# Kernel tuning notes

Measured on AMD Instinct MI355X. Metric: run time of the kernel, lower is better.

## Reference

```python
import jax, jax.numpy as jnp
import numpy as np

B = 2048
F = 267          # frame_size
L = 32           # latent_size
H = 256          # hidden_size (hard-coded in module)
E = 8            # num_experts
G = 64           # gate hidden size (hard-coded)
IN0 = L + F      # decoder layer0 input (latent + frame*cond_frames)
IN1 = L + H      # decoder inter input
OUT = F          # num_future_predictions * frame_size


def _lin_init(key, out_dim, in_dim):
    # kaiming-uniform-like scale
    bound = float(np.sqrt(1.0 / in_dim))
    return jax.random.uniform(key, (out_dim, in_dim), jnp.float32, -bound, bound)


def setup_inputs() -> dict:
    key = jax.random.key(0)
    ks = jax.random.split(key, 24)
    d = {}
    d["x"] = jax.random.normal(ks[0], (B, F), jnp.float32)
    d["c"] = jax.random.normal(ks[1], (B, F), jnp.float32)
    # encoder
    d["fc1_w"] = _lin_init(ks[2], H, 2 * F); d["fc1_b"] = jnp.zeros((H,), jnp.float32)
    d["fc2_w"] = _lin_init(ks[3], H, F + H); d["fc2_b"] = jnp.zeros((H,), jnp.float32)
    d["mu_w"] = _lin_init(ks[4], L, F + H);  d["mu_b"] = jnp.zeros((L,), jnp.float32)
    d["lv_w"] = _lin_init(ks[5], L, F + H);  d["lv_b"] = jnp.zeros((L,), jnp.float32)
    # gate
    d["g0_w"] = _lin_init(ks[6], G, IN0); d["g0_b"] = jnp.zeros((G,), jnp.float32)
    d["g1_w"] = _lin_init(ks[7], G, G);   d["g1_b"] = jnp.zeros((G,), jnp.float32)
    d["g2_w"] = _lin_init(ks[8], E, G);   d["g2_b"] = jnp.zeros((E,), jnp.float32)
    # expert weights [E, in, out], biases [E, out], bias filled 0.01 as in module
    d["w0"] = jax.random.uniform(ks[9], (E, IN0, H), jnp.float32, -1, 1) * np.sqrt(1.0 / IN0)
    d["b0"] = jnp.full((E, H), 0.01, jnp.float32)
    d["w1"] = jax.random.uniform(ks[10], (E, IN1, H), jnp.float32, -1, 1) * np.sqrt(1.0 / IN1)
    d["b1"] = jnp.full((E, H), 0.01, jnp.float32)
    d["w2"] = jax.random.uniform(ks[11], (E, IN1, OUT), jnp.float32, -1, 1) * np.sqrt(1.0 / IN1)
    d["b2"] = jnp.full((E, OUT), 0.01, jnp.float32)
    return d


def reference(x, c, fc1_w, fc1_b, fc2_w, fc2_b, mu_w, mu_b, lv_w, lv_b,
              g0_w, g0_b, g1_w, g1_b, g2_w, g2_b, w0, b0, w1, b1, w2, b2):
    elu = jax.nn.elu
    # ---- encoder ----
    h1 = elu(jnp.concatenate([x, c], axis=1) @ fc1_w.T + fc1_b)
    h2 = elu(jnp.concatenate([x, h1], axis=1) @ fc2_w.T + fc2_b)
    s = jnp.concatenate([x, h2], axis=1)
    mu = s @ mu_w.T + mu_b
    logvar = s @ lv_w.T + lv_b
    eps = jax.random.normal(jax.random.key(42), mu.shape, mu.dtype)
    z = mu + eps * jnp.exp(0.5 * logvar)
    # ---- mixed decoder ----
    g = elu(jnp.concatenate([z, c], axis=1) @ g0_w.T + g0_b)
    g = elu(g @ g1_w.T + g1_b)
    coeff = jax.nn.softmax(g @ g2_w.T + g2_b, axis=1)  # [B, E]
    layer_out = c
    for (W, bvec, act) in ((w0, b0, True), (w1, b1, True), (w2, b2, False)):
        inp = jnp.concatenate([z, layer_out], axis=1)          # [B, in]
        # per-expert GEMM then coefficient mixing (same math as per-sample
        # mixed-weight bmm: coeff @ flat_weight then baddbmm)
        out = jnp.einsum('be,bi,eio->bo', coeff, inp, W, optimize=True)
        out = out + coeff @ bvec                               # mixed bias
        layer_out = elu(out) if act else out
    return (layer_out, mu, logvar)
```

## Files before the change

### kernel.cpp

```cpp
#include <hip/hip_runtime.h>
#include <math.h>
#include <stdint.h>

#define DI __device__ __forceinline__

typedef __attribute__((ext_vector_type(8))) short bf16x8;
typedef __attribute__((ext_vector_type(4))) float f32x4;
typedef __attribute__((ext_vector_type(4))) int i32x4;

DI float elu_f(float v) { return v > 0.f ? v : expm1f(v); }

DI unsigned short f2bf(float f) {
  uint32_t u = __float_as_uint(f);
  return (unsigned short)((u + 0x7FFFu + ((u >> 16) & 1u)) >> 16);
}

DI void threefry2x32(uint32_t k0, uint32_t k1, uint32_t& x0, uint32_t& x1) {
  uint32_t ks0 = k0, ks1 = k1, ks2 = k0 ^ k1 ^ 0x1BD11BDAu;
  x0 += ks0; x1 += ks1;
#define TFR(r) { x0 += x1; x1 = (x1 << r) | (x1 >> (32 - r)); x1 ^= x0; }
  TFR(13) TFR(15) TFR(26) TFR(6)   x0 += ks1; x1 += ks2 + 1u;
  TFR(17) TFR(29) TFR(16) TFR(24)  x0 += ks2; x1 += ks0 + 2u;
  TFR(13) TFR(15) TFR(26) TFR(6)   x0 += ks0; x1 += ks1 + 3u;
  TFR(17) TFR(29) TFR(16) TFR(24)  x0 += ks1; x1 += ks2 + 4u;
  TFR(13) TFR(15) TFR(26) TFR(6)   x0 += ks2; x1 += ks0 + 5u;
#undef TFR
}

DI float erfinv_f(float x) {
  float w = -logf((1.0f - x) * (1.0f + x));
  float p;
  if (w < 5.0f) {
    w -= 2.5f;
    p = 2.81022636e-08f;
    p = fmaf(p, w, 3.43273939e-07f);
    p = fmaf(p, w, -3.5233877e-06f);
    p = fmaf(p, w, -4.39150654e-06f);
    p = fmaf(p, w, 0.00021858087f);
    p = fmaf(p, w, -0.00125372503f);
    p = fmaf(p, w, -0.00417768164f);
    p = fmaf(p, w, 0.246640727f);
    p = fmaf(p, w, 1.50140941f);
  } else {
    w = sqrtf(w) - 3.0f;
    p = -0.000200214257f;
    p = fmaf(p, w, 0.000100950558f);
    p = fmaf(p, w, 0.00134934322f);
    p = fmaf(p, w, -0.00367342844f);
    p = fmaf(p, w, 0.00573950773f);
    p = fmaf(p, w, -0.0076224613f);
    p = fmaf(p, w, 0.00943887047f);
    p = fmaf(p, w, 1.00167406f);
    p = fmaf(p, w, 2.83297682f);
  }
  return p * x;
}

struct MegaArgs {
  const float *x, *c;
  const float *fc1w, *fc1b, *fc2w, *fc2b, *muw, *mub, *lvw, *lvb;
  const float *g0w, *g0b, *g1w, *g1b, *g2w, *g2b;
  const float *w0, *b0, *w1, *b1, *w2, *b2;
  unsigned short *Ax, *Axh, *Axh2, *A0, *A1, *A2;
  unsigned short *fc1t, *fc2t, *mlvt, *g0t, *g1t, *w0b, *w1b, *w2b;
  float *cf, *outY, *outMu, *outLv;
};

template <int KT, int NE, int D, bool ELU, bool OUTF32>
__global__ __launch_bounds__(128, 2)
void pipe16(const unsigned short* __restrict__ A,
            const unsigned short* __restrict__ Wt, int N,
            const float* __restrict__ bias,
            const float* __restrict__ cfp,
            unsigned short* __restrict__ Cb, int ldcb, int cb_off,
            float* __restrict__ Cf) {
  constexpr int Kp = KT * 32, TT = NE * KT;
  __shared__ float bias_s[NE * 16];
  __shared__ float cfs[(NE > 1) ? 256 : 1];
  const int tid = threadIdx.x, lane = tid & 63, wid = tid >> 6;
  const int q = lane >> 4, l16 = lane & 15;
  const int m0 = blockIdx.x * 32, n0 = blockIdx.y * 16;
  const int gc = n0 + l16;
  const int wrow = (gc < N) ? gc : (N - 1);
  const unsigned short* wlane = Wt + (size_t)wrow * Kp + q * 8;
  const unsigned short* alane = A + (size_t)(m0 + wid * 16 + l16) * Kp + q * 8;

  bf16x8 ring[D];
#pragma unroll
  for (int g = 0; g < D; g++) {
    if (g < TT) {
      int e = g / KT, c = g % KT;
      ring[g] = *(const bf16x8*)(wlane + (size_t)e * N * Kp + c * 32);
    }
  }
  bf16x8 areg[KT];
#pragma unroll
  for (int c = 0; c < KT; c++) areg[c] = *(const bf16x8*)(alane + c * 32);

  if (NE == 1) {
    if (tid < 16) bias_s[tid] = (n0 + tid < N) ? bias[n0 + tid] : 0.f;
  } else {
    if (tid < NE * 16) {
      int e = tid >> 4, col = tid & 15;
      bias_s[tid] = (n0 + col < N) ? bias[(size_t)e * N + n0 + col] : 0.f;
    }
    for (int idx = tid; idx < 256; idx += 128)
      cfs[idx] = cfp[(size_t)(m0 + (idx >> 3)) * 8 + (idx & 7)];
  }
  __syncthreads();

  f32x4 acc = {0.f, 0.f, 0.f, 0.f}, accF = {0.f, 0.f, 0.f, 0.f};
#pragma unroll
  for (int g = 0; g < TT; g++) {
    const int e = g / KT, c = g % KT;
    acc = __builtin_amdgcn_mfma_f32_16x16x32_bf16(areg[c], ring[g % D], acc, 0, 0, 0);
    if (g + D < TT) {
      int e2 = (g + D) / KT, c2 = (g + D) % KT;
      ring[g % D] = *(const bf16x8*)(wlane + (size_t)e2 * N * Kp + c2 * 32);
    }
    if (NE > 1 && c == KT - 1) {
      float bv2 = bias_s[e * 16 + l16];
#pragma unroll
      for (int r = 0; r < 4; r++) {
        float ce = cfs[(wid * 16 + q * 4 + r) * 8 + e];
        accF[r] += ce * (acc[r] + bv2);
        acc[r] = 0.f;
      }
    }
  }

  if (gc < N) {
#pragma unroll
    for (int r = 0; r < 4; r++) {
      int row = m0 + wid * 16 + q * 4 + r;
      float v = (NE > 1) ? accF[r] : (acc[r] + bias_s[l16]);
      if (ELU) v = elu_f(v);
      if (OUTF32) Cf[(size_t)row * 267 + gc] = v;
      else Cb[(size_t)row * ldcb + cb_off + gc] = f2bf(v);
    }
  }
}

__global__ __launch_bounds__(256) void k_prep(MegaArgs a) {
  __shared__ __align__(16) unsigned short T[64][72];
  const int bb = blockIdx.x, tid = threadIdx.x;
  if (bb < 512) {
    for (int rr = 0; rr < 4; rr++) {
      int b = bb * 4 + rr;
      const float* xr = a.x + (size_t)b * 267;
      const float* cr = a.c + (size_t)b * 267;
      unsigned short* axr = a.Ax + (size_t)b * 544;
      for (int k = tid; k < 544; k += 256) {
        float v = (k < 267) ? xr[k] : ((k < 534) ? cr[k - 267] : 0.f);
        axr[k] = f2bf(v);
      }
      unsigned short* ahr = a.Axh + (size_t)b * 544;
      unsigned short* ah2 = a.Axh2 + (size_t)b * 544;
      for (int k = tid; k < 267; k += 256) { unsigned short v = f2bf(xr[k]); ahr[k] = v; ah2[k] = v; }
      for (int k = 523 + tid; k < 544; k += 256) { ahr[k] = 0; ah2[k] = 0; }
      unsigned short* a0r = a.A0 + (size_t)b * 320;
      for (int k = tid; k < 288; k += 256)
        a0r[32 + k] = (k < 267) ? f2bf(cr[k]) : (unsigned short)0;
    }
  } else if (bb < 1152) {
    int r = bb - 512;
    const float* src; unsigned short* dst; int Ks, Kp2;
    if (r < 256)      { src = a.fc1w + (size_t)r * 534; dst = a.fc1t + (size_t)r * 544; Ks = 534; Kp2 = 544; }
    else if (r < 512) { int n = r - 256; src = a.fc2w + (size_t)n * 523; dst = a.fc2t + (size_t)n * 544; Ks = 523; Kp2 = 544; }
    else if (r < 576) { int n = r - 512; src = (n < 32) ? (a.muw + (size_t)n * 523) : (a.lvw + (size_t)(n - 32) * 523);
                        dst = a.mlvt + (size_t)n * 544; Ks = 523; Kp2 = 544; }
    else              { int n = r - 576; src = a.g0w + (size_t)n * 299; dst = a.g0t + (size_t)n * 320; Ks = 299; Kp2 = 320; }
    for (int k = tid; k < Kp2; k += 256) dst[k] = (k < Ks) ? f2bf(src[k]) : (unsigned short)0;
  } else if (bb == 1152) {
    for (int k = tid; k < 4096; k += 256) a.g1t[k] = f2bf(a.g1w[k]);
  } else {
    int t = bb - 1153;
    const float* W; unsigned short* D; int K, N2, Kp2, ldW, e, kt, nt;
    if (t < 160)      { e = t / 20;  int lt = t % 20;  kt = lt / 4; nt = lt % 4; W = a.w0; D = a.w0b; K = 299; N2 = 256; Kp2 = 320; ldW = 256; }
    else if (t < 320) { int u = t - 160; e = u / 20; int lt = u % 20; kt = lt / 4; nt = lt % 4; W = a.w1; D = a.w1b; K = 288; N2 = 256; Kp2 = 288; ldW = 256; }
    else              { int u = t - 320; e = u / 25; int lt = u % 25; kt = lt / 5; nt = lt % 5; W = a.w2; D = a.w2b; K = 288; N2 = 267; Kp2 = 288; ldW = 267; }
    const int k0 = kt * 64, n0 = nt * 64;
    const float* We = W + (size_t)e * K * ldW;
    const int jj = tid & 63, ii0 = tid >> 6;
#pragma unroll
    for (int p = 0; p < 16; p++) {
      int i = ii0 + p * 4;
      int gk = k0 + i, gn = n0 + jj;
      float v = (gk < K && gn < N2) ? We[(size_t)gk * ldW + gn] : 0.f;
      T[jj][i] = f2bf(v);
    }
    __syncthreads();
    int j = tid >> 2, chb = tid & 3;
    int gn = n0 + j;
    if (gn < N2) {
      unsigned short* drow = D + ((size_t)e * N2 + gn) * Kp2 + k0;
#pragma unroll
      for (int s = 0; s < 2; s++) {
        int ch = chb + s * 4;
        if (k0 + ch * 8 < Kp2) {
          i32x4 v = *(i32x4*)(&T[j][ch * 8]);
          *(i32x4*)(drow + ch * 8) = v;
        }
      }
    }
  }
}

__global__ __launch_bounds__(256, 2) void k_mulv_gate(MegaArgs a) {
  __shared__ float mlvS[16 * 65];
  __shared__ __align__(16) unsigned short A0p[16 * 328];
  __shared__ __align__(16) unsigned short gaB[16 * 72];
  __shared__ __align__(16) unsigned short g1B[64 * 72];
  __shared__ float g2wT[64 * 8];
  __shared__ float gB[16 * 65];
  __shared__ float lg[16 * 8];
  const int tid = threadIdx.x, lane = tid & 63, wid = tid >> 6;
  const int q = lane >> 4, l16 = lane & 15;
  const int m0 = blockIdx.x * 16;
  const int cl = wid * 16 + l16;

  const unsigned short* alane = a.Axh2 + (size_t)(m0 + l16) * 544 + q * 8;
  const unsigned short* wlA = a.mlvt + (size_t)cl * 544 + q * 8;
  bf16x8 ring[8];
#pragma unroll
  for (int g = 0; g < 8; g++) ring[g] = *(const bf16x8*)(wlA + g * 32);
  bf16x8 areg[17];
#pragma unroll
  for (int c = 0; c < 17; c++) areg[c] = *(const bf16x8*)(alane + c * 32);
  f32x4 acc = {0.f, 0.f, 0.f, 0.f};
#pragma unroll
  for (int g = 0; g < 17; g++) {
    acc = __builtin_amdgcn_mfma_f32_16x16x32_bf16(areg[g], ring[g % 8], acc, 0, 0, 0);
    if (g + 8 < 17) ring[g % 8] = *(const bf16x8*)(wlA + (g + 8) * 32);
  }
#pragma unroll
  for (int r = 0; r < 4; r++) mlvS[(q * 4 + r) * 65 + cl] = acc[r];
  for (int idx = tid; idx < 576; idx += 256) {
    int row = idx / 36, ch = 4 + idx % 36;
    *(i32x4*)(A0p + row * 328 + ch * 8) =
        *(const i32x4*)(a.A0 + (size_t)(m0 + row) * 320 + ch * 8);
  }
  if (tid < 16) { i32x4 z4 = {0, 0, 0, 0}; *(i32x4*)(A0p + tid * 328 + 320) = z4; }
  for (int idx = tid; idx < 512; idx += 256) {
    int row = idx >> 3, ch = idx & 7;
    *(i32x4*)(g1B + row * 72 + ch * 8) = *(const i32x4*)(a.g1t + (size_t)row * 64 + ch * 8);
  }
  for (int idx = tid; idx < 512; idx += 256)
    g2wT[(idx & 63) * 8 + (idx >> 6)] = a.g2w[idx];
  __syncthreads();

  {
    const int m = tid >> 4, j0 = (tid & 15) * 2, R = m0 + m;
#pragma unroll
    for (int jj = 0; jj < 2; jj++) {
      int j = j0 + jj;
      float mu = mlvS[m * 65 + j] + a.mub[j];
      float lvv = mlvS[m * 65 + j + 32] + a.lvb[j];
      uint32_t x0 = 0u, x1 = (uint32_t)(R * 32 + j);
      threefry2x32(0u, 42u, x0, x1);
      uint32_t bits = x0 ^ x1;
      float f = __uint_as_float((bits >> 9) | 0x3F800000u) - 1.0f;
      const float lo = -0.99999994039535522461f;
      float u = fmaf(f, 2.0f, lo);
      u = fmaxf(u, lo);
      float eps = 1.41421356237f * erfinv_f(u);
      float z = fmaf(eps, expf(0.5f * lvv), mu);
      a.outMu[(size_t)R * 32 + j] = mu;
      a.outLv[(size_t)R * 32 + j] = lvv;
      unsigned short zb = f2bf(z);
      A0p[m * 328 + j] = zb;
      a.A0[(size_t)R * 320 + j] = zb;
      a.A1[(size_t)R * 288 + j] = zb;
      a.A2[(size_t)R * 288 + j] = zb;
    }
  }
  __syncthreads();

  const unsigned short* wlC = a.g0t + (size_t)cl * 320 + q * 8;
  bf16x8 ring2[8];
#pragma unroll
  for (int g = 0; g < 8; g++) ring2[g] = *(const bf16x8*)(wlC + g * 32);
  f32x4 accC = {0.f, 0.f, 0.f, 0.f};
#pragma unroll
  for (int g = 0; g < 10; g++) {
    bf16x8 av = *(const bf16x8*)(A0p + l16 * 328 + g * 32 + q * 8);
    accC = __builtin_amdgcn_mfma_f32_16x16x32_bf16(av, ring2[g % 8], accC, 0, 0, 0);
    if (g + 8 < 10) ring2[g % 8] = *(const bf16x8*)(wlC + (g + 8) * 32);
  }
  {
    float bc = a.g0b[cl];
#pragma unroll
    for (int r = 0; r < 4; r++)
      gaB[(q * 4 + r) * 72 + cl] = f2bf(elu_f(accC[r] + bc));
  }
  __syncthreads();

  f32x4 accD = {0.f, 0.f, 0.f, 0.f};
#pragma unroll
  for (int tau = 0; tau < 2; tau++) {
    bf16x8 av = *(const bf16x8*)(gaB + l16 * 72 + tau * 32 + q * 8);
    bf16x8 bv = *(const bf16x8*)(g1B + cl * 72 + tau * 32 + q * 8);
    accD = __builtin_amdgcn_mfma_f32_16x16x32_bf16(av, bv, accD, 0, 0, 0);
  }
  {
    float bc = a.g1b[cl];
#pragma unroll
    for (int r = 0; r < 4; r++)
      gB[(q * 4 + r) * 65 + cl] = elu_f(accD[r] + bc);
  }
  __syncthreads();

  if (tid < 128) {
    int r = tid >> 3, e = tid & 7;
    float d = a.g2b[e];
#pragma unroll 8
    for (int k = 0; k < 64; k++) d = fmaf(gB[r * 65 + k], g2wT[k * 8 + e], d);
    lg[r * 8 + e] = d;
  }
  __syncthreads();
  if (tid < 16) {
    float mx = lg[tid * 8];
#pragma unroll
    for (int e2 = 1; e2 < 8; e2++) mx = fmaxf(mx, lg[tid * 8 + e2]);
    float s = 0.f, ex[8];
#pragma unroll
    for (int e2 = 0; e2 < 8; e2++) { ex[e2] = expf(lg[tid * 8 + e2] - mx); s += ex[e2]; }
    float inv = 1.f / s;
#pragma unroll
    for (int e2 = 0; e2 < 8; e2++) a.cf[(size_t)(m0 + tid) * 8 + e2] = ex[e2] * inv;
  }
}

extern "C" void kernel_launch(void* const* d_in, const int* in_sizes, int n_in,
                              void* d_out, int out_size, void* d_ws, size_t ws_size,
                              hipStream_t stream) {
  (void)in_sizes; (void)n_in; (void)out_size; (void)ws_size;
  float* out = (float*)d_out;
  float* ws = (float*)d_ws;

  MegaArgs a;
  a.x    = (const float*)d_in[0];
  a.c    = (const float*)d_in[1];
  a.fc1w = (const float*)d_in[2];  a.fc1b = (const float*)d_in[3];
  a.fc2w = (const float*)d_in[4];  a.fc2b = (const float*)d_in[5];
  a.muw  = (const float*)d_in[6];  a.mub  = (const float*)d_in[7];
  a.lvw  = (const float*)d_in[8];  a.lvb  = (const float*)d_in[9];
  a.g0w  = (const float*)d_in[10]; a.g0b  = (const float*)d_in[11];
  a.g1w  = (const float*)d_in[12]; a.g1b  = (const float*)d_in[13];
  a.g2w  = (const float*)d_in[14]; a.g2b  = (const float*)d_in[15];
  a.w0   = (const float*)d_in[16]; a.b0   = (const float*)d_in[17];
  a.w1   = (const float*)d_in[18]; a.b1   = (const float*)d_in[19];
  a.w2   = (const float*)d_in[20]; a.b2   = (const float*)d_in[21];

  a.outY  = out;
  a.outMu = out + 2048 * 267;
  a.outLv = a.outMu + 2048 * 32;

  a.Ax   = (unsigned short*)(ws);
  a.Axh  = (unsigned short*)(ws + 557056);
  a.Axh2 = (unsigned short*)(ws + 1114112);
  a.A0   = (unsigned short*)(ws + 1671168);
  a.A1   = (unsigned short*)(ws + 1998848);
  a.A2   = (unsigned short*)(ws + 2293760);
  a.fc1t = (unsigned short*)(ws + 2588672);
  a.fc2t = (unsigned short*)(ws + 2658304);
  a.mlvt = (unsigned short*)(ws + 2727936);
  a.g0t  = (unsigned short*)(ws + 2745344);
  a.g1t  = (unsigned short*)(ws + 2755584);
  a.w0b  = (unsigned short*)(ws + 2757632);
  a.w1b  = (unsigned short*)(ws + 3085312);
  a.w2b  = (unsigned short*)(ws + 3380224);
  a.cf   = ws + 3687808;

  dim3 blkP(256), blkG(128);
  k_prep<<<1673, blkP, 0, stream>>>(a);
  pipe16<17, 1, 12, true, false><<<dim3(64, 16), blkG, 0, stream>>>(
      a.Ax, a.fc1t, 256, a.fc1b, nullptr, a.Axh, 544, 267, nullptr);
  pipe16<17, 1, 12, true, false><<<dim3(64, 16), blkG, 0, stream>>>(
      a.Axh, a.fc2t, 256, a.fc2b, nullptr, a.Axh2, 544, 267, nullptr);
  k_mulv_gate<<<128, blkP, 0, stream>>>(a);
  pipe16<10, 8, 16, true, false><<<dim3(64, 16), blkG, 0, stream>>>(
      a.A0, a.w0b, 256, a.b0, a.cf, a.A1, 288, 32, nullptr);
  pipe16<9, 8, 16, true, false><<<dim3(64, 16), blkG, 0, stream>>>(
      a.A1, a.w1b, 256, a.b1, a.cf, a.A2, 288, 32, nullptr);
  pipe16<9, 8, 16, false, true><<<dim3(64, 17), blkG, 0, stream>>>(
      a.A2, a.w2b, 267, a.b2, a.cf, nullptr, 0, 0, a.outY);
}
```

Measured before the change: 182.8 us.

## Fuse encoder, gate and expert decoder into one per-row-block kernel

```diff
diff --git a/kernel.cpp b/kernel.cpp
--- a/kernel.cpp
+++ b/kernel.cpp
@@ -61,198 +61,153 @@
   const float *fc1w, *fc1b, *fc2w, *fc2b, *muw, *mub, *lvw, *lvb;
   const float *g0w, *g0b, *g1w, *g1b, *g2w, *g2b;
   const float *w0, *b0, *w1, *b1, *w2, *b2;
-  unsigned short *Ax, *Axh, *Axh2, *A0, *A1, *A2;
   unsigned short *fc1t, *fc2t, *mlvt, *g0t, *g1t, *w0b, *w1b, *w2b;
-  float *cf, *outY, *outMu, *outLv;
+  float *outY, *outMu, *outLv;
 };
 
-template <int KT, int NE, int D, bool ELU, bool OUTF32>
-__global__ __launch_bounds__(128, 2)
-void pipe16(const unsigned short* __restrict__ A,
-            const unsigned short* __restrict__ Wt, int N,
-            const float* __restrict__ bias,
-            const float* __restrict__ cfp,
-            unsigned short* __restrict__ Cb, int ldcb, int cb_off,
-            float* __restrict__ Cf) {
-  constexpr int Kp = KT * 32, TT = NE * KT;
-  __shared__ float bias_s[NE * 16];
-  __shared__ float cfs[(NE > 1) ? 256 : 1];
-  const int tid = threadIdx.x, lane = tid & 63, wid = tid >> 6;
+template <int KT, int NE, int TPW, int MODE>
+DI void seg(int lane,
+            const unsigned short* AL, int ldA,
+            const unsigned short* __restrict__ Wt, int N, int tbase,
+            const float* __restrict__ biasG, const float* cfsL,
+            unsigned short* outB, int ldOB, int coffB,
+            float* outF, int ldOF) {
+  constexpr int Kp = KT * 32, D = 8, TT = TPW * NE * KT;
   const int q = lane >> 4, l16 = lane & 15;
-  const int m0 = blockIdx.x * 32, n0 = blockIdx.y * 16;
-  const int gc = n0 + l16;
-  const int wrow = (gc < N) ? gc : (N - 1);
-  const unsigned short* wlane = Wt + (size_t)wrow * Kp + q * 8;
-  const unsigned short* alane = A + (size_t)(m0 + wid * 16 + l16) * Kp + q * 8;
-
+  bf16x8 areg[KT];
+#pragma unroll
+  for (int c = 0; c < KT; c++)
+    areg[c] = *(const bf16x8*)(AL + l16 * ldA + c * 32 + q * 8);
+  int gc[TPW];
+  const unsigned short* wl[TPW];
+  float br[TPW][NE];
+  float cfr[(NE > 1) ? NE * 4 : 1];
+#pragma unroll
+  for (int t = 0; t < TPW; t++) {
+    gc[t] = tbase + t * 16 + l16;
+    int wr = (gc[t] < N) ? gc[t] : N - 1;
+    wl[t] = Wt + (size_t)wr * Kp + q * 8;
+    if (MODE != 1) {
+#pragma unroll
+      for (int e = 0; e < NE; e++)
+        br[t][e] = (gc[t] < N) ? biasG[(size_t)e * N + gc[t]] : 0.f;
+    }
+  }
+  if (NE > 1) {
+#pragma unroll
+    for (int e = 0; e < NE; e++)
+#pragma unroll
+      for (int r = 0; r < 4; r++)
+        cfr[e * 4 + r] = cfsL[(q * 4 + r) * 8 + e];
+  }
   bf16x8 ring[D];
 #pragma unroll
   for (int g = 0; g < D; g++) {
     if (g < TT) {
-      int e = g / KT, c = g % KT;
-      ring[g] = *(const bf16x8*)(wlane + (size_t)e * N * Kp + c * 32);
-    }
-  }
-  bf16x8 areg[KT];
-#pragma unroll
-  for (int c = 0; c < KT; c++) areg[c] = *(const bf16x8*)(alane + c * 32);
-
-  if (NE == 1) {
-    if (tid < 16) bias_s[tid] = (n0 + tid < N) ? bias[n0 + tid] : 0.f;
-  } else {
-    if (tid < NE * 16) {
-      int e = tid >> 4, col = tid & 15;
-      bias_s[tid] = (n0 + col < N) ? bias[(size_t)e * N + n0 + col] : 0.f;
-    }
-    for (int idx = tid; idx < 256; idx += 128)
-      cfs[idx] = cfp[(size_t)(m0 + (idx >> 3)) * 8 + (idx & 7)];
-  }
-  __syncthreads();
-
-  f32x4 acc = {0.f, 0.f, 0.f, 0.f}, accF = {0.f, 0.f, 0.f, 0.f};
+      int t = g / (NE * KT), e = (g / KT) % NE, c = g % KT;
+      ring[g] = *(const bf16x8*)(wl[t] + (size_t)e * N * Kp + c * 32);
+    }
+  }
+  f32x4 acc[TPW], accF[TPW];
+#pragma unroll
+  for (int t = 0; t < TPW; t++) {
+    acc[t] = {0.f, 0.f, 0.f, 0.f};
+    accF[t] = {0.f, 0.f, 0.f, 0.f};
+  }
 #pragma unroll
   for (int g = 0; g < TT; g++) {
-    const int e = g / KT, c = g % KT;
-    acc = __builtin_amdgcn_mfma_f32_16x16x32_bf16(areg[c], ring[g % D], acc, 0, 0, 0);
+    const int t = g / (NE * KT), e = (g / KT) % NE, c = g % KT;
+    acc[t] = __builtin_amdgcn_mfma_f32_16x16x32_bf16(areg[c], ring[g % D], acc[t], 0, 0, 0);
     if (g + D < TT) {
-      int e2 = (g + D) / KT, c2 = (g + D) % KT;
-      ring[g % D] = *(const bf16x8*)(wlane + (size_t)e2 * N * Kp + c2 * 32);
+      int t2 = (g + D) / (NE * KT), e2 = ((g + D) / KT) % NE, c2 = (g + D) % KT;
+      ring[g % D] = *(const bf16x8*)(wl[t2] + (size_t)e2 * N * Kp + c2 * 32);
     }
     if (NE > 1 && c == KT - 1) {
-      float bv2 = bias_s[e * 16 + l16];
 #pragma unroll
       for (int r = 0; r < 4; r++) {
-        float ce = cfs[(wid * 16 + q * 4 + r) * 8 + e];
-        accF[r] += ce * (acc[r] + bv2);
-        acc[r] = 0.f;
+        accF[t][r] += cfr[e * 4 + r] * (acc[t][r] + br[t][e]);
+        acc[t][r] = 0.f;
       }
     }
   }
-
-  if (gc < N) {
+#pragma unroll
+  for (int t = 0; t < TPW; t++) {
+    if (gc[t] >= N) continue;
 #pragma unroll
     for (int r = 0; r < 4; r++) {
-      int row = m0 + wid * 16 + q * 4 + r;
-      float v = (NE > 1) ? accF[r] : (acc[r] + bias_s[l16]);
-      if (ELU) v = elu_f(v);
-      if (OUTF32) Cf[(size_t)row * 267 + gc] = v;
-      else Cb[(size_t)row * ldcb + cb_off + gc] = f2bf(v);
-    }
-  }
-}
-
-__global__ __launch_bounds__(256) void k_prep(MegaArgs a) {
-  __shared__ __align__(16) unsigned short T[64][72];
-  const int bb = blockIdx.x, tid = threadIdx.x;
-  if (bb < 512) {
-    for (int rr = 0; rr < 4; rr++) {
-      int b = bb * 4 + rr;
-      const float* xr = a.x + (size_t)b * 267;
-      const float* cr = a.c + (size_t)b * 267;
-      unsigned short* axr = a.Ax + (size_t)b * 544;
-      for (int k = tid; k < 544; k += 256) {
-        float v = (k < 267) ? xr[k] : ((k < 534) ? cr[k - 267] : 0.f);
-        axr[k] = f2bf(v);
-      }
-      unsigned short* ahr = a.Axh + (size_t)b * 544;
-      unsigned short* ah2 = a.Axh2 + (size_t)b * 544;
-      for (int k = tid; k < 267; k += 256) { unsigned short v = f2bf(xr[k]); ahr[k] = v; ah2[k] = v; }
-      for (int k = 523 + tid; k < 544; k += 256) { ahr[k] = 0; ah2[k] = 0; }
-      unsigned short* a0r = a.A0 + (size_t)b * 320;
-      for (int k = tid; k < 288; k += 256)
-        a0r[32 + k] = (k < 267) ? f2bf(cr[k]) : (unsigned short)0;
-    }
-  } else if (bb < 1152) {
-    int r = bb - 512;
-    const float* src; unsigned short* dst; int Ks, Kp2;
-    if (r < 256)      { src = a.fc1w + (size_t)r * 534; dst = a.fc1t + (size_t)r * 544; Ks = 534; Kp2 = 544; }
-    else if (r < 512) { int n = r - 256; src = a.fc2w + (size_t)n * 523; dst = a.fc2t + (size_t)n * 544; Ks = 523; Kp2 = 544; }
-    else if (r < 576) { int n = r - 512; src = (n < 32) ? (a.muw + (size_t)n * 523) : (a.lvw + (size_t)(n - 32) * 523);
-                        dst = a.mlvt + (size_t)n * 544; Ks = 523; Kp2 = 544; }
-    else              { int n = r - 576; src = a.g0w + (size_t)n * 299; dst = a.g0t + (size_t)n * 320; Ks = 299; Kp2 = 320; }
-    for (int k = tid; k < Kp2; k += 256) dst[k] = (k < Ks) ? f2bf(src[k]) : (unsigned short)0;
-  } else if (bb == 1152) {
-    for (int k = tid; k < 4096; k += 256) a.g1t[k] = f2bf(a.g1w[k]);
-  } else {
-    int t = bb - 1153;
-    const float* W; unsigned short* D; int K, N2, Kp2, ldW, e, kt, nt;
-    if (t < 160)      { e = t / 20;  int lt = t % 20;  kt = lt / 4; nt = lt % 4; W = a.w0; D = a.w0b; K = 299; N2 = 256; Kp2 = 320; ldW = 256; }
-    else if (t < 320) { int u = t - 160; e = u / 20; int lt = u % 20; kt = lt / 4; nt = lt % 4; W = a.w1; D = a.w1b; K = 288; N2 = 256; Kp2 = 288; ldW = 256; }
-    else              { int u = t - 320; e = u / 25; int lt = u % 25; kt = lt / 5; nt = lt % 5; W = a.w2; D = a.w2b; K = 288; N2 = 267; Kp2 = 288; ldW = 267; }
-    const int k0 = kt * 64, n0 = nt * 64;
-    const float* We = W + (size_t)e * K * ldW;
-    const int jj = tid & 63, ii0 = tid >> 6;
-#pragma unroll
-    for (int p = 0; p < 16; p++) {
-      int i = ii0 + p * 4;
-      int gk = k0 + i, gn = n0 + jj;
-      float v = (gk < K && gn < N2) ? We[(size_t)gk * ldW + gn] : 0.f;
-      T[jj][i] = f2bf(v);
-    }
-    __syncthreads();
-    int j = tid >> 2, chb = tid & 3;
-    int gn = n0 + j;
-    if (gn < N2) {
-      unsigned short* drow = D + ((size_t)e * N2 + gn) * Kp2 + k0;
-#pragma unroll
-      for (int s = 0; s < 2; s++) {
-        int ch = chb + s * 4;
-        if (k0 + ch * 8 < Kp2) {
-          i32x4 v = *(i32x4*)(&T[j][ch * 8]);
-          *(i32x4*)(drow + ch * 8) = v;
-        }
-      }
-    }
-  }
-}
-
-__global__ __launch_bounds__(256, 2) void k_mulv_gate(MegaArgs a) {
-  __shared__ float mlvS[16 * 65];
-  __shared__ __align__(16) unsigned short A0p[16 * 328];
-  __shared__ __align__(16) unsigned short gaB[16 * 72];
-  __shared__ __align__(16) unsigned short g1B[64 * 72];
-  __shared__ float g2wT[64 * 8];
-  __shared__ float gB[16 * 65];
-  __shared__ float lg[16 * 8];
-  const int tid = threadIdx.x, lane = tid & 63, wid = tid >> 6;
-  const int q = lane >> 4, l16 = lane & 15;
+      const int row = q * 4 + r;
+      if (MODE == 0)
+        outB[row * ldOB + coffB + gc[t]] = f2bf(elu_f(acc[t][r] + br[t][0]));
+      else if (MODE == 1)
+        outF[row * ldOF + gc[t]] = acc[t][r];
+      else if (MODE == 4)
+        outF[row * ldOF + gc[t]] = elu_f(acc[t][r] + br[t][0]);
+      else if (MODE == 2)
+        outB[row * ldOB + coffB + gc[t]] = f2bf(elu_f(accF[t][r]));
+      else
+        outF[(size_t)row * ldOF + gc[t]] = accF[t][r];
+    }
+  }
+}
+
+__global__ __launch_bounds__(512, 2) void row_net(MegaArgs a) {
+  __shared__ __align__(16) unsigned char SM[46336];
+  unsigned short* Acat0 = (unsigned short*)SM;
+  unsigned short* Acat1 = (unsigned short*)(SM + 17664);
+  unsigned short* A0p   = (unsigned short*)(SM + 35328);
+  float* cfs = (float*)(SM + 45824);
+  unsigned short* A1p = Acat0;
+  float* gB   = (float*)(SM + 9472);
+  float* lg   = (float*)(SM + 13632);
+  float* g2wT = (float*)(SM + 14144);
+  unsigned short* A2p = Acat1;
+  float* mlvS = (float*)(SM + 17664 + 9472);
+  unsigned short* gaB = (unsigned short*)(SM + 17664 + 13632);
+
+  const int tid = threadIdx.x, lane = tid & 63, wv = tid >> 6;
   const int m0 = blockIdx.x * 16;
-  const int cl = wid * 16 + l16;
-
-  const unsigned short* alane = a.Axh2 + (size_t)(m0 + l16) * 544 + q * 8;
-  const unsigned short* wlA = a.mlvt + (size_t)cl * 544 + q * 8;
-  bf16x8 ring[8];
-#pragma unroll
-  for (int g = 0; g < 8; g++) ring[g] = *(const bf16x8*)(wlA + g * 32);
-  bf16x8 areg[17];
-#pragma unroll
-  for (int c = 0; c < 17; c++) areg[c] = *(const bf16x8*)(alane + c * 32);
-  f32x4 acc = {0.f, 0.f, 0.f, 0.f};
-#pragma unroll
-  for (int g = 0; g < 17; g++) {
-    acc = __builtin_amdgcn_mfma_f32_16x16x32_bf16(areg[g], ring[g % 8], acc, 0, 0, 0);
-    if (g + 8 < 17) ring[g % 8] = *(const bf16x8*)(wlA + (g + 8) * 32);
-  }
-#pragma unroll
-  for (int r = 0; r < 4; r++) mlvS[(q * 4 + r) * 65 + cl] = acc[r];
-  for (int idx = tid; idx < 576; idx += 256) {
-    int row = idx / 36, ch = 4 + idx % 36;
-    *(i32x4*)(A0p + row * 328 + ch * 8) =
-        *(const i32x4*)(a.A0 + (size_t)(m0 + row) * 320 + ch * 8);
-  }
-  if (tid < 16) { i32x4 z4 = {0, 0, 0, 0}; *(i32x4*)(A0p + tid * 328 + 320) = z4; }
-  for (int idx = tid; idx < 512; idx += 256) {
-    int row = idx >> 3, ch = idx & 7;
-    *(i32x4*)(g1B + row * 72 + ch * 8) = *(const i32x4*)(a.g1t + (size_t)row * 64 + ch * 8);
-  }
-  for (int idx = tid; idx < 512; idx += 256)
-    g2wT[(idx & 63) * 8 + (idx >> 6)] = a.g2w[idx];
-  __syncthreads();
-
-  {
-    const int m = tid >> 4, j0 = (tid & 15) * 2, R = m0 + m;
-#pragma unroll
-    for (int jj = 0; jj < 2; jj++) {
+
+  for (int idx = tid; idx < 16 * 267; idx += 512) {
+    int r = idx / 267, k = idx % 267;
+    unsigned short xv = f2bf(a.x[(size_t)(m0 + r) * 267 + k]);
+    Acat0[r * 552 + k] = xv;
+    Acat1[r * 552 + k] = xv;
+    unsigned short cv = f2bf(a.c[(size_t)(m0 + r) * 267 + k]);
+    Acat0[r * 552 + 267 + k] = cv;
+    A0p[r * 328 + 32 + k] = cv;
+  }
+  for (int idx = tid; idx < 16 * 18; idx += 512) {
+    int r = idx / 18, k = idx % 18;
+    Acat0[r * 552 + 534 + k] = 0;
+  }
+  for (int idx = tid; idx < 16 * 29; idx += 512) {
+    int r = idx / 29, k = idx % 29;
+    Acat1[r * 552 + 523 + k] = 0;
+  }
+  for (int idx = tid; idx < 16 * 29; idx += 512) {
+    int r = idx / 29, k = idx % 29;
+    A0p[r * 328 + 299 + k] = 0;
+  }
+  __syncthreads();
+
+  seg<17, 1, 2, 0>(lane, Acat0, 552, a.fc1t, 256, wv * 32, a.fc1b, nullptr,
+                   Acat1, 552, 267, nullptr, 0);
+  __syncthreads();
+  seg<17, 1, 2, 0>(lane, Acat1, 552, a.fc2t, 256, wv * 32, a.fc2b, nullptr,
+                   Acat0, 552, 267, nullptr, 0);
+  for (int idx = tid; idx < 16 * 21; idx += 512) {
+    int r = idx / 21, k = idx % 21;
+    Acat0[r * 552 + 523 + k] = 0;
+  }
+  __syncthreads();
+  if (wv < 4)
+    seg<17, 1, 1, 1>(lane, Acat0, 552, a.mlvt, 64, wv * 16, nullptr, nullptr,
+                     nullptr, 0, 0, mlvS, 65);
+  __syncthreads();
+  if (tid < 128) {
+    const int m = tid >> 3, j0 = (tid & 7) * 4, R = m0 + m;
+#pragma unroll
+    for (int jj = 0; jj < 4; jj++) {
       int j = j0 + jj;
       float mu = mlvS[m * 65 + j] + a.mub[j];
       float lvv = mlvS[m * 65 + j + 32] + a.lvb[j];
@@ -269,47 +224,23 @@
       a.outLv[(size_t)R * 32 + j] = lvv;
       unsigned short zb = f2bf(z);
       A0p[m * 328 + j] = zb;
-      a.A0[(size_t)R * 320 + j] = zb;
-      a.A1[(size_t)R * 288 + j] = zb;
-      a.A2[(size_t)R * 288 + j] = zb;
-    }
-  }
-  __syncthreads();
-
-  const unsigned short* wlC = a.g0t + (size_t)cl * 320 + q * 8;
-  bf16x8 ring2[8];
-#pragma unroll
-  for (int g = 0; g < 8; g++) ring2[g] = *(const bf16x8*)(wlC + g * 32);
-  f32x4 accC = {0.f, 0.f, 0.f, 0.f};
-#pragma unroll
-  for (int g = 0; g < 10; g++) {
-    bf16x8 av = *(const bf16x8*)(A0p + l16 * 328 + g * 32 + q * 8);
-    accC = __builtin_amdgcn_mfma_f32_16x16x32_bf16(av, ring2[g % 8], accC, 0, 0, 0);
-    if (g + 8 < 10) ring2[g % 8] = *(const bf16x8*)(wlC + (g + 8) * 32);
-  }
-  {
-    float bc = a.g0b[cl];
-#pragma unroll
-    for (int r = 0; r < 4; r++)
-      gaB[(q * 4 + r) * 72 + cl] = f2bf(elu_f(accC[r] + bc));
-  }
-  __syncthreads();
-
-  f32x4 accD = {0.f, 0.f, 0.f, 0.f};
-#pragma unroll
-  for (int tau = 0; tau < 2; tau++) {
-    bf16x8 av = *(const bf16x8*)(gaB + l16 * 72 + tau * 32 + q * 8);
-    bf16x8 bv = *(const bf16x8*)(g1B + cl * 72 + tau * 32 + q * 8);
-    accD = __builtin_amdgcn_mfma_f32_16x16x32_bf16(av, bv, accD, 0, 0, 0);
-  }
-  {
-    float bc = a.g1b[cl];
-#pragma unroll
-    for (int r = 0; r < 4; r++)
-      gB[(q * 4 + r) * 65 + cl] = elu_f(accD[r] + bc);
-  }
-  __syncthreads();
-
+      A1p[m * 296 + j] = zb;
+      A2p[m * 296 + j] = zb;
+    }
+  }
+  __syncthreads();
+  if (wv < 4)
+    seg<10, 1, 1, 0>(lane, A0p, 328, a.g0t, 64, wv * 16, a.g0b, nullptr,
+                     gaB, 72, 0, nullptr, 0);
+  if (tid >= 256) {
+    for (int idx = tid - 256; idx < 512; idx += 256)
+      g2wT[(idx & 63) * 8 + (idx >> 6)] = a.g2w[idx];
+  }
+  __syncthreads();
+  if (wv < 4)
+    seg<2, 1, 1, 4>(lane, gaB, 72, a.g1t, 64, wv * 16, a.g1b, nullptr,
+                    nullptr, 0, 0, gB, 65);
+  __syncthreads();
   if (tid < 128) {
     int r = tid >> 3, e = tid & 7;
     float d = a.g2b[e];
@@ -327,7 +258,67 @@
     for (int e2 = 0; e2 < 8; e2++) { ex[e2] = expf(lg[tid * 8 + e2] - mx); s += ex[e2]; }
     float inv = 1.f / s;
 #pragma unroll
-    for (int e2 = 0; e2 < 8; e2++) a.cf[(size_t)(m0 + tid) * 8 + e2] = ex[e2] * inv;
+    for (int e2 = 0; e2 < 8; e2++) cfs[tid * 8 + e2] = ex[e2] * inv;
+  }
+  __syncthreads();
+  seg<10, 8, 2, 2>(lane, A0p, 328, a.w0b, 256, wv * 32, a.b0, cfs,
+                   A1p, 296, 32, nullptr, 0);
+  __syncthreads();
+  seg<9, 8, 2, 2>(lane, A1p, 296, a.w1b, 256, wv * 32, a.b1, cfs,
+                  A2p, 296, 32, nullptr, 0);
+  __syncthreads();
+  float* oY = a.outY + (size_t)m0 * 267;
+  seg<9, 8, 2, 3>(lane, A2p, 296, a.w2b, 267, wv * 32, a.b2, cfs,
+                  nullptr, 0, 0, oY, 267);
+  if (wv == 0)
+    seg<9, 8, 1, 3>(lane, A2p, 296, a.w2b, 267, 256, a.b2, cfs,
+                    nullptr, 0, 0, oY, 267);
+}
+
+__global__ __launch_bounds__(256) void k_prep(MegaArgs a) {
+  __shared__ __align__(16) unsigned short T[64][72];
+  const int bb = blockIdx.x, tid = threadIdx.x;
+  if (bb < 640) {
+    int r = bb;
+    const float* src; unsigned short* dst; int Ks, Kp2;
+    if (r < 256)      { src = a.fc1w + (size_t)r * 534; dst = a.fc1t + (size_t)r * 544; Ks = 534; Kp2 = 544; }
+    else if (r < 512) { int n = r - 256; src = a.fc2w + (size_t)n * 523; dst = a.fc2t + (size_t)n * 544; Ks = 523; Kp2 = 544; }
+    else if (r < 576) { int n = r - 512; src = (n < 32) ? (a.muw + (size_t)n * 523) : (a.lvw + (size_t)(n - 32) * 523);
+                        dst = a.mlvt + (size_t)n * 544; Ks = 523; Kp2 = 544; }
+    else              { int n = r - 576; src = a.g0w + (size_t)n * 299; dst = a.g0t + (size_t)n * 320; Ks = 299; Kp2 = 320; }
+    for (int k = tid; k < Kp2; k += 256) dst[k] = (k < Ks) ? f2bf(src[k]) : (unsigned short)0;
+  } else if (bb == 640) {
+    for (int k = tid; k < 4096; k += 256) a.g1t[k] = f2bf(a.g1w[k]);
+  } else {
+    int t = bb - 641;
+    const float* W; unsigned short* D; int K, N2, Kp2, ldW, e, kt, nt;
+    if (t < 160)      { e = t / 20;  int lt = t % 20;  kt = lt / 4; nt = lt % 4; W = a.w0; D = a.w0b; K = 299; N2 = 256; Kp2 = 320; ldW = 256; }
+    else if (t < 320) { int u = t - 160; e = u / 20; int lt = u % 20; kt = lt / 4; nt = lt % 4; W = a.w1; D = a.w1b; K = 288; N2 = 256; Kp2 = 288; ldW = 256; }
+    else              { int u = t - 320; e = u / 25; int lt = u % 25; kt = lt / 5; nt = lt % 5; W = a.w2; D = a.w2b; K = 288; N2 = 267; Kp2 = 288; ldW = 267; }
+    const int k0 = kt * 64, n0 = nt * 64;
+    const float* We = W + (size_t)e * K * ldW;
+    const int jj = tid & 63, ii0 = tid >> 6;
+#pragma unroll
+    for (int p = 0; p < 16; p++) {
+      int i = ii0 + p * 4;
+      int gk = k0 + i, gn = n0 + jj;
+      float v = (gk < K && gn < N2) ? We[(size_t)gk * ldW + gn] : 0.f;
+      T[jj][i] = f2bf(v);
+    }
+    __syncthreads();
+    int j = tid >> 2, chb = tid & 3;
+    int gn = n0 + j;
+    if (gn < N2) {
+      unsigned short* drow = D + ((size_t)e * N2 + gn) * Kp2 + k0;
+#pragma unroll
+      for (int s = 0; s < 2; s++) {
+        int ch = chb + s * 4;
+        if (k0 + ch * 8 < Kp2) {
+          i32x4 v = *(i32x4*)(&T[j][ch * 8]);
+          *(i32x4*)(drow + ch * 8) = v;
+        }
+      }
+    }
   }
 }
 
@@ -356,33 +347,15 @@
   a.outMu = out + 2048 * 267;
   a.outLv = a.outMu + 2048 * 32;
 
-  a.Ax   = (unsigned short*)(ws);
-  a.Axh  = (unsigned short*)(ws + 557056);
-  a.Axh2 = (unsigned short*)(ws + 1114112);
-  a.A0   = (unsigned short*)(ws + 1671168);
-  a.A1   = (unsigned short*)(ws + 1998848);
-  a.A2   = (unsigned short*)(ws + 2293760);
-  a.fc1t = (unsigned short*)(ws + 2588672);
-  a.fc2t = (unsigned short*)(ws + 2658304);
-  a.mlvt = (unsigned short*)(ws + 2727936);
-  a.g0t  = (unsigned short*)(ws + 2745344);
-  a.g1t  = (unsigned short*)(ws + 2755584);
-  a.w0b  = (unsigned short*)(ws + 2757632);
-  a.w1b  = (unsigned short*)(ws + 3085312);
-  a.w2b  = (unsigned short*)(ws + 3380224);
-  a.cf   = ws + 3687808;
-
-  dim3 blkP(256), blkG(128);
-  k_prep<<<1673, blkP, 0, stream>>>(a);
-  pipe16<17, 1, 12, true, false><<<dim3(64, 16), blkG, 0, stream>>>(
-      a.Ax, a.fc1t, 256, a.fc1b, nullptr, a.Axh, 544, 267, nullptr);
-  pipe16<17, 1, 12, true, false><<<dim3(64, 16), blkG, 0, stream>>>(
-      a.Axh, a.fc2t, 256, a.fc2b, nullptr, a.Axh2, 544, 267, nullptr);
-  k_mulv_gate<<<128, blkP, 0, stream>>>(a);
-  pipe16<10, 8, 16, true, false><<<dim3(64, 16), blkG, 0, stream>>>(
-      a.A0, a.w0b, 256, a.b0, a.cf, a.A1, 288, 32, nullptr);
-  pipe16<9, 8, 16, true, false><<<dim3(64, 16), blkG, 0, stream>>>(
-      a.A1, a.w1b, 256, a.b1, a.cf, a.A2, 288, 32, nullptr);
-  pipe16<9, 8, 16, false, true><<<dim3(64, 17), blkG, 0, stream>>>(
-      a.A2, a.w2b, 267, a.b2, a.cf, nullptr, 0, 0, a.outY);
-}
+  a.fc1t = (unsigned short*)(ws);
+  a.fc2t = (unsigned short*)(ws + 69632);
+  a.mlvt = (unsigned short*)(ws + 139264);
+  a.g0t  = (unsigned short*)(ws + 156672);
+  a.g1t  = (unsigned short*)(ws + 166912);
+  a.w0b  = (unsigned short*)(ws + 168960);
+  a.w1b  = (unsigned short*)(ws + 496640);
+  a.w2b  = (unsigned short*)(ws + 791552);
+
+  k_prep<<<1161, dim3(256), 0, stream>>>(a);
+  row_net<<<128, dim3(512), 0, stream>>>(a);
+}
```

Result: slower. 386.4 us (+111.4%).

## Widen GEMM tile to 32 columns with each weight fragment reused across two row tiles

Applied to the files above, without the earlier changes.

```diff
diff --git a/kernel.cpp b/kernel.cpp
--- a/kernel.cpp
+++ b/kernel.cpp
@@ -68,22 +68,22 @@
 
 template <int KT, int NE, int D, bool ELU, bool OUTF32>
 __global__ __launch_bounds__(128, 2)
-void pipe16(const unsigned short* __restrict__ A,
+void pipe32(const unsigned short* __restrict__ A,
             const unsigned short* __restrict__ Wt, int N,
             const float* __restrict__ bias,
             const float* __restrict__ cfp,
             unsigned short* __restrict__ Cb, int ldcb, int cb_off,
             float* __restrict__ Cf) {
   constexpr int Kp = KT * 32, TT = NE * KT;
-  __shared__ float bias_s[NE * 16];
+  __shared__ float bias_s[NE * 32];
   __shared__ float cfs[(NE > 1) ? 256 : 1];
-  const int tid = threadIdx.x, lane = tid & 63, wid = tid >> 6;
+  const int tid = threadIdx.x, lane = tid & 63, wv = tid >> 6;
   const int q = lane >> 4, l16 = lane & 15;
-  const int m0 = blockIdx.x * 32, n0 = blockIdx.y * 16;
+  const int m0 = blockIdx.x * 32;
+  const int n0 = blockIdx.y * 32 + wv * 16;
   const int gc = n0 + l16;
   const int wrow = (gc < N) ? gc : (N - 1);
   const unsigned short* wlane = Wt + (size_t)wrow * Kp + q * 8;
-  const unsigned short* alane = A + (size_t)(m0 + wid * 16 + l16) * Kp + q * 8;
 
   bf16x8 ring[D];
 #pragma unroll
@@ -93,51 +93,65 @@
       ring[g] = *(const bf16x8*)(wlane + (size_t)e * N * Kp + c * 32);
     }
   }
-  bf16x8 areg[KT];
-#pragma unroll
-  for (int c = 0; c < KT; c++) areg[c] = *(const bf16x8*)(alane + c * 32);
+  bf16x8 areg[2][KT];
+#pragma unroll
+  for (int t = 0; t < 2; t++) {
+    const unsigned short* alane = A + (size_t)(m0 + t * 16 + l16) * Kp + q * 8;
+#pragma unroll
+    for (int c = 0; c < KT; c++) areg[t][c] = *(const bf16x8*)(alane + c * 32);
+  }
 
   if (NE == 1) {
-    if (tid < 16) bias_s[tid] = (n0 + tid < N) ? bias[n0 + tid] : 0.f;
+    if (tid < 32) {
+      int col = blockIdx.y * 32 + tid;
+      bias_s[tid] = (col < N) ? bias[col] : 0.f;
+    }
   } else {
-    if (tid < NE * 16) {
-      int e = tid >> 4, col = tid & 15;
-      bias_s[tid] = (n0 + col < N) ? bias[(size_t)e * N + n0 + col] : 0.f;
+    for (int idx = tid; idx < NE * 32; idx += 128) {
+      int e = idx >> 5, col = blockIdx.y * 32 + (idx & 31);
+      bias_s[idx] = (col < N) ? bias[(size_t)e * N + col] : 0.f;
     }
     for (int idx = tid; idx < 256; idx += 128)
       cfs[idx] = cfp[(size_t)(m0 + (idx >> 3)) * 8 + (idx & 7)];
   }
   __syncthreads();
 
-  f32x4 acc = {0.f, 0.f, 0.f, 0.f}, accF = {0.f, 0.f, 0.f, 0.f};
+  f32x4 acc[2] = {{0.f, 0.f, 0.f, 0.f}, {0.f, 0.f, 0.f, 0.f}};
+  f32x4 accF[2] = {{0.f, 0.f, 0.f, 0.f}, {0.f, 0.f, 0.f, 0.f}};
 #pragma unroll
   for (int g = 0; g < TT; g++) {
     const int e = g / KT, c = g % KT;
-    acc = __builtin_amdgcn_mfma_f32_16x16x32_bf16(areg[c], ring[g % D], acc, 0, 0, 0);
+    bf16x8 bv = ring[g % D];
+    acc[0] = __builtin_amdgcn_mfma_f32_16x16x32_bf16(areg[0][c], bv, acc[0], 0, 0, 0);
+    acc[1] = __builtin_amdgcn_mfma_f32_16x16x32_bf16(areg[1][c], bv, acc[1], 0, 0, 0);
     if (g + D < TT) {
       int e2 = (g + D) / KT, c2 = (g + D) % KT;
       ring[g % D] = *(const bf16x8*)(wlane + (size_t)e2 * N * Kp + c2 * 32);
     }
     if (NE > 1 && c == KT - 1) {
-      float bv2 = bias_s[e * 16 + l16];
+      float bv2 = bias_s[e * 32 + wv * 16 + l16];
+#pragma unroll
+      for (int t = 0; t < 2; t++)
+#pragma unroll
+        for (int r = 0; r < 4; r++) {
+          float ce = cfs[(t * 16 + q * 4 + r) * 8 + e];
+          accF[t][r] += ce * (acc[t][r] + bv2);
+          acc[t][r] = 0.f;
+        }
+    }
+  }
+
+  if (gc < N) {
+#pragma unroll
+    for (int t = 0; t < 2; t++)
 #pragma unroll
       for (int r = 0; r < 4; r++) {
-        float ce = cfs[(wid * 16 + q * 4 + r) * 8 + e];
-        accF[r] += ce * (acc[r] + bv2);
-        acc[r] = 0.f;
+        int row = m0 + t * 16 + q * 4 + r;
+        float v = (NE > 1) ? accF[t][r] : (acc[t][r] + bias_s[wv * 16 + l16]);
+        if (ELU) v = elu_f(v);
+        if (OUTF32) Cf[(size_t)row * 267 + gc] = v;
+        else Cb[(size_t)row * ldcb + cb_off + gc] = f2bf(v);
       }
-    }
-  }
-
-  if (gc < N) {
-#pragma unroll
-    for (int r = 0; r < 4; r++) {
-      int row = m0 + wid * 16 + q * 4 + r;
-      float v = (NE > 1) ? accF[r] : (acc[r] + bias_s[l16]);
-      if (ELU) v = elu_f(v);
-      if (OUTF32) Cf[(size_t)row * 267 + gc] = v;
-      else Cb[(size_t)row * ldcb + cb_off + gc] = f2bf(v);
-    }
   }
 }
 
@@ -374,15 +388,15 @@
 
   dim3 blkP(256), blkG(128);
   k_prep<<<1673, blkP, 0, stream>>>(a);
-  pipe16<17, 1, 12, true, false><<<dim3(64, 16), blkG, 0, stream>>>(
+  pipe32<17, 1, 12, true, false><<<dim3(64, 8), blkG, 0, stream>>>(
       a.Ax, a.fc1t, 256, a.fc1b, nullptr, a.Axh, 544, 267, nullptr);
-  pipe16<17, 1, 12, true, false><<<dim3(64, 16), blkG, 0, stream>>>(
+  pipe32<17, 1, 12, true, false><<<dim3(64, 8), blkG, 0, stream>>>(
       a.Axh, a.fc2t, 256, a.fc2b, nullptr, a.Axh2, 544, 267, nullptr);
   k_mulv_gate<<<128, blkP, 0, stream>>>(a);
-  pipe16<10, 8, 16, true, false><<<dim3(64, 16), blkG, 0, stream>>>(
+  pipe32<10, 8, 12, true, false><<<dim3(64, 8), blkG, 0, stream>>>(
       a.A0, a.w0b, 256, a.b0, a.cf, a.A1, 288, 32, nullptr);
-  pipe16<9, 8, 16, true, false><<<dim3(64, 16), blkG, 0, stream>>>(
+  pipe32<9, 8, 12, true, false><<<dim3(64, 8), blkG, 0, stream>>>(
       a.A1, a.w1b, 256, a.b1, a.cf, a.A2, 288, 32, nullptr);
-  pipe16<9, 8, 16, false, true><<<dim3(64, 17), blkG, 0, stream>>>(
+  pipe32<9, 8, 12, false, true><<<dim3(64, 9), blkG, 0, stream>>>(
       a.A2, a.w2b, 267, a.b2, a.cf, nullptr, 0, 0, a.outY);
 }
```

Measured after the change: 175.6 us. 1.04x faster.
